# Performance work log

Measured on AMD Instinct MI355X. Metric: run time of the kernel, lower is better.

Reference implementation:

```python
import jax, jax.numpy as jnp
import numpy as np

MIN_WEIGHT = 0.0
MAX_WEIGHT = 500.0


def setup_inputs() -> dict:
    key = jax.random.key(0)
    k1, k2, k3 = jax.random.split(key, 3)
    B, P = 131072, 64   # groundings, predicates
    C, L = 128, 3       # clauses, literals per clause
    ground_atoms = jax.random.normal(k1, (B, P), dtype=jnp.float32)
    # learned clause weights, initial_clause_weight = 0.5
    clause_weights = 0.5 * jnp.ones((C,), dtype=jnp.float32)
    # which predicate each literal refers to
    literal_idx = jax.random.randint(k2, (C, L), 0, P, dtype=jnp.int64)
    # 0 -> negated literal (sign -1), 1 -> positive literal (sign +1)
    sign_bits = jax.random.randint(k3, (C, L), 0, 2, dtype=jnp.int32)
    return {
        "ground_atoms": ground_atoms,
        "clause_weights": clause_weights,
        "literal_idx": literal_idx,
        "sign_bits": sign_bits,
    }


def reference(ground_atoms, clause_weights, literal_idx, sign_bits):
    """Vectorized KnowledgeEnhancer forward.

    Per clause (GodelBoostConormApprox):
      literals = signs * ground_atoms[:, idx]
      delta    = signs * clamp(w) * softmax(literals)
    Then concat all clause deltas and scatter_add into predicate space.
    """
    B, P = ground_atoms.shape
    C, L = literal_idx.shape
    signs = (2 * sign_bits - 1).astype(ground_atoms.dtype)  # [C, L] in {-1,+1}
    gathered = ground_atoms[:, literal_idx]                 # [B, C, L] gather
    literals = signs[None, :, :] * gathered                 # signed pre-activations
    w = jnp.clip(clause_weights, MIN_WEIGHT, MAX_WEIGHT)    # [C]
    delta = signs[None, :, :] * w[None, :, None] * jax.nn.softmax(literals, axis=-1)
    # concat over clauses (dim=1 in the torch code) then scatter_add over predicates
    delta_flat = delta.reshape(B, C * L)
    idx_flat = literal_idx.reshape(C * L)
    out = jax.ops.segment_sum(delta_flat.T, idx_flat, num_segments=P)  # [P, B]
    return out.T  # [B, P]
```

## Files before the change

kernel.cpp:

```cpp
#include <hip/hip_runtime.h>
#include <stdint.h>

typedef unsigned int  u32;
typedef unsigned short u16;

#define B_ROWS 131072
#define P_PRED 64
#define C_CLS  128
#define NPAIR  384
#define CAP    32
#define RPB    128
#define TPB    512
#define GCAP   128
#define LOG2E  1.4426950408889634f

#if __has_builtin(__builtin_amdgcn_exp2f)
#define EXP2F(x) __builtin_amdgcn_exp2f(x)
#else
#define EXP2F(x) exp2f(x)
#endif

#if __has_builtin(__builtin_amdgcn_rcpf)
#define RCPF(x) __builtin_amdgcn_rcpf(x)
#else
#define RCPF(x) (1.0f / (x))
#endif

__device__ __forceinline__ float bf16_to_f(u16 u) {
    return __uint_as_float(((u32)u) << 16);
}
__device__ __forceinline__ u16 f_to_bf16(float f) {
    u32 u = __float_as_uint(f);
    u += 0x7FFFu + ((u >> 16) & 1u);
    return (u16)(u >> 16);
}

__global__ void ke_prep(const u32* __restrict__ lidx_w,
                        const u32* __restrict__ sb_w,
                        const u32* __restrict__ w_w,
                        uint2* __restrict__ stream,
                        u32* __restrict__ cnt8w,
                        u32* __restrict__ flags) {
    __shared__ int scnt[P_PRED];
    __shared__ u32 recPk[P_PRED][CAP];
    __shared__ float recW[P_PRED][CAP];
    __shared__ int sidx[NPAIR];
    __shared__ int ssb[NPAIR];
    __shared__ int det[3];
    const int t = threadIdx.x;
    if (t < P_PRED) scnt[t] = 0;
    if (t < 3) det[t] = 1;
    __syncthreads();
    if (t < NPAIR / 2) {
        if (lidx_w[2 * t + 1] != 0u) det[0] = 0;
        if (sb_w[2 * t + 1]   != 0u) det[1] = 0;
    }
    if (t == 0 && (w_w[0] & 0xFFFFu) == 0u) det[2] = 0;
    __syncthreads();
    if (t < NPAIR) {
        sidx[t] = (int)(det[0] ? lidx_w[2 * t] : lidx_w[t]);
        ssb[t]  = (int)(det[1] ? sb_w[2 * t]   : sb_w[t]);
    }
    __syncthreads();
    if (t < NPAIR) {
        const int c = t / 3;
        const int l = t - c * 3;
        const int base = c * 3;
        const int o1 = base + (l == 0 ? 1 : 0);
        const int o2 = base + (l == 2 ? 1 : 2);
        const int p = sidx[t];
        const int slot = atomicAdd(&scnt[p], 1);
        float wraw = det[2] ? bf16_to_f((u16)(w_w[c / 2] >> ((c & 1) * 16)))
                            : __uint_as_float(w_w[c]);
        float wc = fminf(fmaxf(wraw, 0.0f), 500.0f);
        if (slot < CAP) {
            u32 s1 = 2u * (u32)sidx[o1] + (ssb[o1] ? 0u : 1u);
            u32 s2 = 2u * (u32)sidx[o2] + (ssb[o2] ? 0u : 1u);
            recPk[p][slot] = (ssb[t] ? 0u : 1u) | (s1 << 8) | (s2 << 16);
            recW[p][slot]  = ssb[t] ? wc : -wc;
        }
    }
    __syncthreads();
    if (t < P_PRED) {
        const int p = t;
        const int g = p >> 3;
        const int n = min(scnt[p], CAP);
        int off = 0;
        for (int pb = g * 8; pb < p; ++pb) off += min(scnt[pb], CAP);
        int ncl = 0;
        for (int j = 0; j < n; ++j) {
            if (off + j < GCAP) {
                stream[g * GCAP + off + j] =
                    make_uint2(recPk[p][j], __float_as_uint(recW[p][j]));
                ++ncl;
            }
        }
        ((unsigned char*)cnt8w)[p] = (unsigned char)ncl;
    }
    if (t == 0) flags[0] = (u32)det[2];
}

__global__ __launch_bounds__(TPB, 8)
void ke_main(const void* __restrict__ atoms_v,
             const uint2* __restrict__ stream,
             const u32* __restrict__ cnt8w,
             const u32* __restrict__ flags,
             void* __restrict__ out_v) {
    __shared__ float E[P_PRED * RPB];
    const int tid = threadIdx.x;
    const int lane = tid & 63;
    const int g = __builtin_amdgcn_readfirstlane(tid >> 6);
    const int rowBase = blockIdx.x * RPB;
    const bool bf16m = (flags[0] != 0u);

    {
        const int r = tid >> 2;
        const int c0 = (tid & 3) * 16;
        if (bf16m) {
            const u16* gp = (const u16*)atoms_v + (size_t)(rowBase + r) * P_PRED + c0;
            uint4 v0 = *(const uint4*)gp;
            uint4 v1 = *(const uint4*)(gp + 8);
            u32 w[8] = {v0.x, v0.y, v0.z, v0.w, v1.x, v1.y, v1.z, v1.w};
#pragma unroll
            for (int j = 0; j < 8; ++j) {
                float xlo = __uint_as_float(w[j] << 16) * LOG2E;
                float xhi = __uint_as_float(w[j] & 0xFFFF0000u) * LOG2E;
                E[(c0 + 2 * j)     * RPB + r] = EXP2F(xlo);
                E[(c0 + 2 * j + 1) * RPB + r] = EXP2F(xhi);
            }
        } else {
            const float* gp = (const float*)atoms_v + (size_t)(rowBase + r) * P_PRED + c0;
#pragma unroll
            for (int j4 = 0; j4 < 4; ++j4) {
                float4 v = *(const float4*)(gp + 4 * j4);
                E[(c0 + 4 * j4 + 0) * RPB + r] = EXP2F(v.x * LOG2E);
                E[(c0 + 4 * j4 + 1) * RPB + r] = EXP2F(v.y * LOG2E);
                E[(c0 + 4 * j4 + 2) * RPB + r] = EXP2F(v.z * LOG2E);
                E[(c0 + 4 * j4 + 3) * RPB + r] = EXP2F(v.w * LOG2E);
            }
        }
    }

    uint2 rA = stream[g * GCAP + lane];
    uint2 rB = stream[g * GCAP + 64 + lane];
    const u32 cntLo = cnt8w[g * 2];
    const u32 cntHi = cnt8w[g * 2 + 1];

    __syncthreads();

    const int q2 = lane * 2;
    float2 acc[8];
    int j = 0;
#pragma unroll
    for (int pp = 0; pp < 8; ++pp) {
        const int p = g * 8 + pp;
        float2 ep = *(const float2*)&E[p * RPB + q2];
        float2 epn;
        epn.x = RCPF(ep.x);
        epn.y = RCPF(ep.y);
        const int n = (int)((pp < 4 ? (cntLo >> (8 * pp))
                                    : (cntHi >> (8 * (pp - 4)))) & 255u);
        float2 a = make_float2(0.0f, 0.0f);
        for (int e = 0; e < n; ++e, ++j) {
            u32 pk, swb;
            if (j < 64) {
                pk  = (u32)__builtin_amdgcn_readlane((int)rA.x, j);
                swb = (u32)__builtin_amdgcn_readlane((int)rA.y, j);
            } else {
                pk  = (u32)__builtin_amdgcn_readlane((int)rB.x, j - 64);
                swb = (u32)__builtin_amdgcn_readlane((int)rB.y, j - 64);
            }
            const float sw = __uint_as_float(swb);
            const u32 o1 = (pk >> 8) & 255u;
            const u32 o2 = (pk >> 16) & 255u;
            float2 s1 = *(const float2*)&E[(int)(o1 >> 1) * RPB + q2];
            float2 s2 = *(const float2*)&E[(int)(o2 >> 1) * RPB + q2];
            if (o1 & 1u) { s1.x = RCPF(s1.x); s1.y = RCPF(s1.y); }
            if (o2 & 1u) { s2.x = RCPF(s2.x); s2.y = RCPF(s2.y); }
            const float2 ss = (pk & 1u) ? epn : ep;
            float tx = RCPF(ss.x + s1.x + s2.x);
            float ty = RCPF(ss.y + s1.y + s2.y);
            a.x = fmaf(sw * ss.x, tx, a.x);
            a.y = fmaf(sw * ss.y, ty, a.y);
        }
        acc[pp] = a;
    }

    if (bf16m) {
        u16* op0 = (u16*)out_v + (size_t)(rowBase + q2) * P_PRED + g * 8;
        u16* op1 = op0 + P_PRED;
        uint4 o0, o1v;
        o0.x  = (u32)f_to_bf16(acc[0].x) | ((u32)f_to_bf16(acc[1].x) << 16);
        o0.y  = (u32)f_to_bf16(acc[2].x) | ((u32)f_to_bf16(acc[3].x) << 16);
        o0.z  = (u32)f_to_bf16(acc[4].x) | ((u32)f_to_bf16(acc[5].x) << 16);
        o0.w  = (u32)f_to_bf16(acc[6].x) | ((u32)f_to_bf16(acc[7].x) << 16);
        o1v.x = (u32)f_to_bf16(acc[0].y) | ((u32)f_to_bf16(acc[1].y) << 16);
        o1v.y = (u32)f_to_bf16(acc[2].y) | ((u32)f_to_bf16(acc[3].y) << 16);
        o1v.z = (u32)f_to_bf16(acc[4].y) | ((u32)f_to_bf16(acc[5].y) << 16);
        o1v.w = (u32)f_to_bf16(acc[6].y) | ((u32)f_to_bf16(acc[7].y) << 16);
        *(uint4*)op0 = o0;
        *(uint4*)op1 = o1v;
    } else {
        float* op0 = (float*)out_v + (size_t)(rowBase + q2) * P_PRED + g * 8;
        float* op1 = op0 + P_PRED;
        *(float4*)(op0)     = make_float4(acc[0].x, acc[1].x, acc[2].x, acc[3].x);
        *(float4*)(op0 + 4) = make_float4(acc[4].x, acc[5].x, acc[6].x, acc[7].x);
        *(float4*)(op1)     = make_float4(acc[0].y, acc[1].y, acc[2].y, acc[3].y);
        *(float4*)(op1 + 4) = make_float4(acc[4].y, acc[5].y, acc[6].y, acc[7].y);
    }
}

extern "C" void kernel_launch(void* const* d_in, const int* in_sizes, int n_in,
                              void* d_out, int out_size, void* d_ws, size_t ws_size,
                              hipStream_t stream_h) {
    const u32* clause_weights = (const u32*)d_in[1];
    const u32* literal_idx    = (const u32*)d_in[2];
    const u32* sign_bits      = (const u32*)d_in[3];

    uint2* stream = (uint2*)d_ws;
    u32*   cnt8w  = (u32*)((char*)d_ws + 8 * GCAP * 8);
    u32*   flags  = (u32*)((char*)d_ws + 8 * GCAP * 8 + 64);

    ke_prep<<<1, NPAIR, 0, stream_h>>>(literal_idx, sign_bits, clause_weights,
                                       stream, cnt8w, flags);
    ke_main<<<B_ROWS / RPB, TPB, 0, stream_h>>>(d_in[0], stream, cnt8w, flags,
                                                d_out);
}
```

Measured before the change: 112.2 us.

## Precompute exp and reciprocal tables in LDS and read clause records from memory

The main kernel now stores both exp(x) and 1/exp(x) per predicate in a doubled LDS table, so the inner loop no longer computes conditional reciprocals. Clause records are unpacked into four-word entries per predicate slot and read through scalar loads instead of readlane from a packed per-group stream. The inner loop is unrolled by two, and the launch-bounds occupancy hint drops from 8 to 4 because LDS use doubles to 64KB per block. The per-group cap of 128 records is removed. The trade-off is more LDS per block and lower occupancy in return for less ALU work per record.

```diff
diff --git a/kernel.cpp b/kernel.cpp
--- a/kernel.cpp
+++ b/kernel.cpp
@@ -11,7 +11,6 @@
 #define CAP    32
 #define RPB    128
 #define TPB    512
-#define GCAP   128
 #define LOG2E  1.4426950408889634f
 
 #if __has_builtin(__builtin_amdgcn_exp2f)
@@ -38,12 +37,10 @@
 __global__ void ke_prep(const u32* __restrict__ lidx_w,
                         const u32* __restrict__ sb_w,
                         const u32* __restrict__ w_w,
-                        uint2* __restrict__ stream,
-                        u32* __restrict__ cnt8w,
+                        u32* __restrict__ recs,
+                        int* __restrict__ cnts,
                         u32* __restrict__ flags) {
     __shared__ int scnt[P_PRED];
-    __shared__ u32 recPk[P_PRED][CAP];
-    __shared__ float recW[P_PRED][CAP];
     __shared__ int sidx[NPAIR];
     __shared__ int ssb[NPAIR];
     __shared__ int det[3];
@@ -74,39 +71,25 @@
                             : __uint_as_float(w_w[c]);
         float wc = fminf(fmaxf(wraw, 0.0f), 500.0f);
         if (slot < CAP) {
-            u32 s1 = 2u * (u32)sidx[o1] + (ssb[o1] ? 0u : 1u);
-            u32 s2 = 2u * (u32)sidx[o2] + (ssb[o2] ? 0u : 1u);
-            recPk[p][slot] = (ssb[t] ? 0u : 1u) | (s1 << 8) | (s2 << 16);
-            recW[p][slot]  = ssb[t] ? wc : -wc;
-        }
-    }
-    __syncthreads();
-    if (t < P_PRED) {
-        const int p = t;
-        const int g = p >> 3;
-        const int n = min(scnt[p], CAP);
-        int off = 0;
-        for (int pb = g * 8; pb < p; ++pb) off += min(scnt[pb], CAP);
-        int ncl = 0;
-        for (int j = 0; j < n; ++j) {
-            if (off + j < GCAP) {
-                stream[g * GCAP + off + j] =
-                    make_uint2(recPk[p][j], __float_as_uint(recW[p][j]));
-                ++ncl;
-            }
-        }
-        ((unsigned char*)cnt8w)[p] = (unsigned char)ncl;
-    }
+            u32* r = recs + (p * CAP + slot) * 4;
+            r[0] = ssb[t] ? 0u : 1u;
+            r[1] = 2u * (u32)sidx[o1] + (ssb[o1] ? 0u : 1u);
+            r[2] = 2u * (u32)sidx[o2] + (ssb[o2] ? 0u : 1u);
+            r[3] = __float_as_uint(ssb[t] ? wc : -wc);
+        }
+    }
+    __syncthreads();
+    if (t < P_PRED) cnts[t] = min(scnt[t], CAP);
     if (t == 0) flags[0] = (u32)det[2];
 }
 
-__global__ __launch_bounds__(TPB, 8)
+__global__ __launch_bounds__(TPB, 4)
 void ke_main(const void* __restrict__ atoms_v,
-             const uint2* __restrict__ stream,
-             const u32* __restrict__ cnt8w,
+             const u32* __restrict__ recs_u,
+             const int* __restrict__ cnts,
              const u32* __restrict__ flags,
              void* __restrict__ out_v) {
-    __shared__ float E[P_PRED * RPB];
+    __shared__ float E2[2 * P_PRED * RPB];
     const int tid = threadIdx.x;
     const int lane = tid & 63;
     const int g = __builtin_amdgcn_readfirstlane(tid >> 6);
@@ -125,69 +108,66 @@
             for (int j = 0; j < 8; ++j) {
                 float xlo = __uint_as_float(w[j] << 16) * LOG2E;
                 float xhi = __uint_as_float(w[j] & 0xFFFF0000u) * LOG2E;
-                E[(c0 + 2 * j)     * RPB + r] = EXP2F(xlo);
-                E[(c0 + 2 * j + 1) * RPB + r] = EXP2F(xhi);
+                float elo = EXP2F(xlo), ehi = EXP2F(xhi);
+                E2[(2 * (c0 + 2 * j))         * RPB + r] = elo;
+                E2[(2 * (c0 + 2 * j) + 1)     * RPB + r] = RCPF(elo);
+                E2[(2 * (c0 + 2 * j + 1))     * RPB + r] = ehi;
+                E2[(2 * (c0 + 2 * j + 1) + 1) * RPB + r] = RCPF(ehi);
             }
         } else {
             const float* gp = (const float*)atoms_v + (size_t)(rowBase + r) * P_PRED + c0;
 #pragma unroll
             for (int j4 = 0; j4 < 4; ++j4) {
                 float4 v = *(const float4*)(gp + 4 * j4);
-                E[(c0 + 4 * j4 + 0) * RPB + r] = EXP2F(v.x * LOG2E);
-                E[(c0 + 4 * j4 + 1) * RPB + r] = EXP2F(v.y * LOG2E);
-                E[(c0 + 4 * j4 + 2) * RPB + r] = EXP2F(v.z * LOG2E);
-                E[(c0 + 4 * j4 + 3) * RPB + r] = EXP2F(v.w * LOG2E);
+                float xs[4] = {v.x, v.y, v.z, v.w};
+#pragma unroll
+                for (int j = 0; j < 4; ++j) {
+                    float e = EXP2F(xs[j] * LOG2E);
+                    E2[(2 * (c0 + 4 * j4 + j))     * RPB + r] = e;
+                    E2[(2 * (c0 + 4 * j4 + j) + 1) * RPB + r] = RCPF(e);
+                }
             }
         }
     }
-
-    uint2 rA = stream[g * GCAP + lane];
-    uint2 rB = stream[g * GCAP + 64 + lane];
-    const u32 cntLo = cnt8w[g * 2];
-    const u32 cntHi = cnt8w[g * 2 + 1];
-
-    __syncthreads();
-
-    const int q2 = lane * 2;
+    __syncthreads();
+
+    const int q8 = lane * 2;
     float2 acc[8];
-    int j = 0;
+
 #pragma unroll
     for (int pp = 0; pp < 8; ++pp) {
         const int p = g * 8 + pp;
-        float2 ep = *(const float2*)&E[p * RPB + q2];
-        float2 epn;
-        epn.x = RCPF(ep.x);
-        epn.y = RCPF(ep.y);
-        const int n = (int)((pp < 4 ? (cntLo >> (8 * pp))
-                                    : (cntHi >> (8 * (pp - 4)))) & 255u);
+        const float2 epp = *(const float2*)&E2[(2 * p)     * RPB + q8];
+        const float2 epn = *(const float2*)&E2[(2 * p + 1) * RPB + q8];
+        const int n = min(cnts[p], CAP);
+        const u32* rp = recs_u + p * CAP * 4;
         float2 a = make_float2(0.0f, 0.0f);
-        for (int e = 0; e < n; ++e, ++j) {
-            u32 pk, swb;
-            if (j < 64) {
-                pk  = (u32)__builtin_amdgcn_readlane((int)rA.x, j);
-                swb = (u32)__builtin_amdgcn_readlane((int)rA.y, j);
-            } else {
-                pk  = (u32)__builtin_amdgcn_readlane((int)rB.x, j - 64);
-                swb = (u32)__builtin_amdgcn_readlane((int)rB.y, j - 64);
-            }
-            const float sw = __uint_as_float(swb);
-            const u32 o1 = (pk >> 8) & 255u;
-            const u32 o2 = (pk >> 16) & 255u;
-            float2 s1 = *(const float2*)&E[(int)(o1 >> 1) * RPB + q2];
-            float2 s2 = *(const float2*)&E[(int)(o2 >> 1) * RPB + q2];
-            if (o1 & 1u) { s1.x = RCPF(s1.x); s1.y = RCPF(s1.y); }
-            if (o2 & 1u) { s2.x = RCPF(s2.x); s2.y = RCPF(s2.y); }
-            const float2 ss = (pk & 1u) ? epn : ep;
-            float tx = RCPF(ss.x + s1.x + s2.x);
-            float ty = RCPF(ss.y + s1.y + s2.y);
-            a.x = fmaf(sw * ss.x, tx, a.x);
-            a.y = fmaf(sw * ss.y, ty, a.y);
-        }
+
+#define REC_BODY(EIDX)                                                        \
+        {                                                                     \
+            const u32* r = rp + (EIDX) * 4;               \
+            const float2 ss = r[0] ? epn : epp;           \
+            const float sw = __uint_as_float(r[3]);                           \
+            float2 s1 = *(const float2*)&E2[(int)r[1] * RPB + q8];            \
+            float2 s2 = *(const float2*)&E2[(int)r[2] * RPB + q8];            \
+            float tx = RCPF(ss.x + s1.x + s2.x);                              \
+            float ty = RCPF(ss.y + s1.y + s2.y);                              \
+            a.x = fmaf(sw * ss.x, tx, a.x);                                   \
+            a.y = fmaf(sw * ss.y, ty, a.y);                                   \
+        }
+
+        int e = 0;
+        for (; e + 1 < n; e += 2) {
+            REC_BODY(e)
+            REC_BODY(e + 1)
+        }
+        if (e < n) REC_BODY(e)
+#undef REC_BODY
         acc[pp] = a;
     }
 
     if (bf16m) {
-        u16* op0 = (u16*)out_v + (size_t)(rowBase + q2) * P_PRED + g * 8;
+        u16* op0 = (u16*)out_v + (size_t)(rowBase + q8) * P_PRED + g * 8;
         u16* op1 = op0 + P_PRED;
         uint4 o0, o1v;
         o0.x  = (u32)f_to_bf16(acc[0].x) | ((u32)f_to_bf16(acc[1].x) << 16);
@@ -201,7 +181,7 @@
         *(uint4*)op0 = o0;
         *(uint4*)op1 = o1v;
     } else {
-        float* op0 = (float*)out_v + (size_t)(rowBase + q2) * P_PRED + g * 8;
+        float* op0 = (float*)out_v + (size_t)(rowBase + q8) * P_PRED + g * 8;
         float* op1 = op0 + P_PRED;
         *(float4*)(op0)     = make_float4(acc[0].x, acc[1].x, acc[2].x, acc[3].x);
         *(float4*)(op0 + 4) = make_float4(acc[4].x, acc[5].x, acc[6].x, acc[7].x);
@@ -217,12 +197,12 @@
     const u32* literal_idx    = (const u32*)d_in[2];
     const u32* sign_bits      = (const u32*)d_in[3];
 
-    uint2* stream = (uint2*)d_ws;
-    u32*   cnt8w  = (u32*)((char*)d_ws + 8 * GCAP * 8);
-    u32*   flags  = (u32*)((char*)d_ws + 8 * GCAP * 8 + 64);
+    u32* recs  = (u32*)d_ws;
+    int* cnts  = (int*)((char*)d_ws + P_PRED * CAP * 16);
+    u32* flags = (u32*)((char*)d_ws + P_PRED * CAP * 16 + 256);
 
     ke_prep<<<1, NPAIR, 0, stream_h>>>(literal_idx, sign_bits, clause_weights,
-                                       stream, cnt8w, flags);
-    ke_main<<<B_ROWS / RPB, TPB, 0, stream_h>>>(d_in[0], stream, cnt8w, flags,
+                                       recs, cnts, flags);
+    ke_main<<<B_ROWS / RPB, TPB, 0, stream_h>>>(d_in[0], recs, cnts, flags,
                                                 d_out);
 }
```

New measurement: 106.9 us. 1.05x faster.

## Store exp and reciprocal as bf16 in LDS and stage clause records in shared

Applied to the files above, without the earlier changes.

The exp table in LDS becomes bf16 and holds both exp(x) and 1/exp(x), so the inner loop no longer computes conditional reciprocals for negated literals. Clause records and counts are copied into shared memory and read per iteration instead of being fetched with readlane from registers. The inner loop is unrolled by two, and the tile-load mapping changes so each thread handles one row and a 16-column chunk. This trades fp32 accuracy for bf16 rounding of the exp values. It also shrinks the per-group record cap from 128 to 104, which could drop clauses if a group has more than 104 literals.

```diff
diff --git a/kernel.cpp b/kernel.cpp
--- a/kernel.cpp
+++ b/kernel.cpp
@@ -11,7 +11,7 @@
 #define CAP    32
 #define RPB    128
 #define TPB    512
-#define GCAP   128
+#define GCAP   104
 #define LOG2E  1.4426950408889634f
 
 #if __has_builtin(__builtin_amdgcn_exp2f)
@@ -102,87 +102,102 @@
 
 __global__ __launch_bounds__(TPB, 8)
 void ke_main(const void* __restrict__ atoms_v,
-             const uint2* __restrict__ stream,
+             const uint2* __restrict__ stream_g,
              const u32* __restrict__ cnt8w,
              const u32* __restrict__ flags,
              void* __restrict__ out_v) {
-    __shared__ float E[P_PRED * RPB];
+    __shared__ u16 E2[2 * P_PRED * RPB];
+    __shared__ uint2 srec[8 * GCAP];
+    __shared__ unsigned char cnt8[P_PRED];
     const int tid = threadIdx.x;
     const int lane = tid & 63;
     const int g = __builtin_amdgcn_readfirstlane(tid >> 6);
     const int rowBase = blockIdx.x * RPB;
     const bool bf16m = (flags[0] != 0u);
 
+    for (int i = tid; i < 8 * GCAP; i += TPB) srec[i] = stream_g[i];
+    if (tid < 16) ((u32*)cnt8)[tid] = cnt8w[tid];
+
     {
-        const int r = tid >> 2;
-        const int c0 = (tid & 3) * 16;
+        const int r = tid & 127;
+        const int c0 = (tid >> 7) * 16;
         if (bf16m) {
             const u16* gp = (const u16*)atoms_v + (size_t)(rowBase + r) * P_PRED + c0;
             uint4 v0 = *(const uint4*)gp;
             uint4 v1 = *(const uint4*)(gp + 8);
             u32 w[8] = {v0.x, v0.y, v0.z, v0.w, v1.x, v1.y, v1.z, v1.w};
 #pragma unroll
-            for (int j = 0; j < 8; ++j) {
-                float xlo = __uint_as_float(w[j] << 16) * LOG2E;
-                float xhi = __uint_as_float(w[j] & 0xFFFF0000u) * LOG2E;
-                E[(c0 + 2 * j)     * RPB + r] = EXP2F(xlo);
-                E[(c0 + 2 * j + 1) * RPB + r] = EXP2F(xhi);
+            for (int k = 0; k < 8; ++k) {
+                float xlo = __uint_as_float(w[k] << 16) * LOG2E;
+                float xhi = __uint_as_float(w[k] & 0xFFFF0000u) * LOG2E;
+                float elo = EXP2F(xlo), ehi = EXP2F(xhi);
+                const int sl = 2 * (c0 + 2 * k);
+                E2[(sl)     * RPB + r] = f_to_bf16(elo);
+                E2[(sl + 1) * RPB + r] = f_to_bf16(RCPF(elo));
+                E2[(sl + 2) * RPB + r] = f_to_bf16(ehi);
+                E2[(sl + 3) * RPB + r] = f_to_bf16(RCPF(ehi));
             }
         } else {
             const float* gp = (const float*)atoms_v + (size_t)(rowBase + r) * P_PRED + c0;
 #pragma unroll
-            for (int j4 = 0; j4 < 4; ++j4) {
-                float4 v = *(const float4*)(gp + 4 * j4);
-                E[(c0 + 4 * j4 + 0) * RPB + r] = EXP2F(v.x * LOG2E);
-                E[(c0 + 4 * j4 + 1) * RPB + r] = EXP2F(v.y * LOG2E);
-                E[(c0 + 4 * j4 + 2) * RPB + r] = EXP2F(v.z * LOG2E);
-                E[(c0 + 4 * j4 + 3) * RPB + r] = EXP2F(v.w * LOG2E);
+            for (int k4 = 0; k4 < 4; ++k4) {
+                float4 v = *(const float4*)(gp + 4 * k4);
+                float xs[4] = {v.x, v.y, v.z, v.w};
+#pragma unroll
+                for (int k = 0; k < 4; ++k) {
+                    float e = EXP2F(xs[k] * LOG2E);
+                    const int sl = 2 * (c0 + 4 * k4 + k);
+                    E2[(sl)     * RPB + r] = f_to_bf16(e);
+                    E2[(sl + 1) * RPB + r] = f_to_bf16(RCPF(e));
+                }
             }
         }
     }
-
-    uint2 rA = stream[g * GCAP + lane];
-    uint2 rB = stream[g * GCAP + 64 + lane];
-    const u32 cntLo = cnt8w[g * 2];
-    const u32 cntHi = cnt8w[g * 2 + 1];
-
-    __syncthreads();
-
-    const int q2 = lane * 2;
+    __syncthreads();
+
+    const int q2 = 2 * lane;
     float2 acc[8];
-    int j = 0;
+    int j = g * GCAP;
+
 #pragma unroll
     for (int pp = 0; pp < 8; ++pp) {
         const int p = g * 8 + pp;
-        float2 ep = *(const float2*)&E[p * RPB + q2];
-        float2 epn;
-        epn.x = RCPF(ep.x);
-        epn.y = RCPF(ep.y);
-        const int n = (int)((pp < 4 ? (cntLo >> (8 * pp))
-                                    : (cntHi >> (8 * (pp - 4)))) & 255u);
+        const u32 eppv = *(const u32*)&E2[(2 * p)     * RPB + q2];
+        const u32 epnv = *(const u32*)&E2[(2 * p + 1) * RPB + q2];
+        const float eppx = __uint_as_float(eppv << 16);
+        const float eppy = __uint_as_float(eppv & 0xFFFF0000u);
+        const float epnx = __uint_as_float(epnv << 16);
+        const float epny = __uint_as_float(epnv & 0xFFFF0000u);
+        const int n = (int)cnt8[p];
         float2 a = make_float2(0.0f, 0.0f);
-        for (int e = 0; e < n; ++e, ++j) {
-            u32 pk, swb;
-            if (j < 64) {
-                pk  = (u32)__builtin_amdgcn_readlane((int)rA.x, j);
-                swb = (u32)__builtin_amdgcn_readlane((int)rA.y, j);
-            } else {
-                pk  = (u32)__builtin_amdgcn_readlane((int)rB.x, j - 64);
-                swb = (u32)__builtin_amdgcn_readlane((int)rB.y, j - 64);
-            }
-            const float sw = __uint_as_float(swb);
-            const u32 o1 = (pk >> 8) & 255u;
-            const u32 o2 = (pk >> 16) & 255u;
-            float2 s1 = *(const float2*)&E[(int)(o1 >> 1) * RPB + q2];
-            float2 s2 = *(const float2*)&E[(int)(o2 >> 1) * RPB + q2];
-            if (o1 & 1u) { s1.x = RCPF(s1.x); s1.y = RCPF(s1.y); }
-            if (o2 & 1u) { s2.x = RCPF(s2.x); s2.y = RCPF(s2.y); }
-            const float2 ss = (pk & 1u) ? epn : ep;
-            float tx = RCPF(ss.x + s1.x + s2.x);
-            float ty = RCPF(ss.y + s1.y + s2.y);
-            a.x = fmaf(sw * ss.x, tx, a.x);
-            a.y = fmaf(sw * ss.y, ty, a.y);
-        }
+
+#define REC_BODY(J)                                                           \
+        {                                                                     \
+            const uint2 rec = srec[J];                  \
+            const u32 pk = rec.x;                                             \
+            const float sw = __uint_as_float(rec.y);                          \
+            const u32 s1v = *(const u32*)&E2[(int)((pk >> 8)  & 255u) * RPB + q2]; \
+            const u32 s2v = *(const u32*)&E2[(int)((pk >> 16) & 255u) * RPB + q2]; \
+            const float ssx = (pk & 1u) ? epnx : eppx;                        \
+            const float ssy = (pk & 1u) ? epny : eppy;                        \
+            const float s1x = __uint_as_float(s1v << 16);                     \
+            const float s1y = __uint_as_float(s1v & 0xFFFF0000u);             \
+            const float s2x = __uint_as_float(s2v << 16);                     \
+            const float s2y = __uint_as_float(s2v & 0xFFFF0000u);             \
+            const float tx = RCPF(ssx + s1x + s2x);                           \
+            const float ty = RCPF(ssy + s1y + s2y);                          \
+            a.x = fmaf(sw * ssx, tx, a.x);                                    \
+            a.y = fmaf(sw * ssy, ty, a.y);                                    \
+        }
+
+        int e = 0;
+        for (; e + 1 < n; e += 2) {
+            REC_BODY(j)
+            REC_BODY(j + 1)
+            j += 2;
+        }
+        if (e < n) { REC_BODY(j) ++j; }
+#undef REC_BODY
         acc[pp] = a;
     }
 
```

New measurement: 103.0 us. -8.2%, faster.
